# Kernel optimization log

Hardware: AMD Instinct MI355X
Metric: run time of the kernel (lower is better)

The kernel has to match this reference:

```python
import jax, jax.numpy as jnp
import numpy as np

B, L, D_MODEL = 2, 2048, 2048
D_INNER, D_STATE, D_CONV, DT_RANK = 4096, 16, 4, 128


def setup_inputs() -> dict:
    key = jax.random.key(0)
    ks = jax.random.split(key, 8)
    s = 0.02
    return {
        "hidden_states": jax.random.normal(ks[0], (B, L, D_MODEL), jnp.float32),
        "in_proj_weight": jax.random.normal(ks[1], (2 * D_INNER, D_MODEL), jnp.float32) * s,
        "conv1d_weight": jax.random.normal(ks[2], (D_INNER, 1, D_CONV), jnp.float32) * s,
        "conv1d_bias": jnp.zeros((D_INNER,), jnp.float32),
        "x_proj_weight": jax.random.normal(ks[3], (DT_RANK + 2 * D_STATE, D_INNER), jnp.float32) * s,
        "dt_proj_weight": jax.random.normal(ks[4], (D_INNER, DT_RANK), jnp.float32) * s,
        "dt_proj_bias": jax.random.uniform(ks[5], (D_INNER,), jnp.float32, -4.0, -2.0),
        "out_proj_weight": jax.random.normal(ks[6], (D_MODEL, D_INNER), jnp.float32) * s,
        # real Mamba init: A_log = log(1..d_state) broadcast over channels
        "A_log": jnp.log(jnp.broadcast_to(jnp.arange(1, D_STATE + 1, dtype=jnp.float32), (D_INNER, D_STATE))),
        "D": jnp.ones((D_INNER,), jnp.float32),
    }


def reference(hidden_states, in_proj_weight, conv1d_weight, conv1d_bias,
              x_proj_weight, dt_proj_weight, dt_proj_bias, out_proj_weight,
              A_log, D):
    negA = -jnp.exp(A_log)  # [d_inner, d_state]
    # in_proj (no bias) then transpose(1,2): [B, 2*d_inner, L]
    xz = jnp.einsum('bld,ed->bel', hidden_states, in_proj_weight)
    x, z = jnp.split(xz, 2, axis=1)  # each [B, d_inner, L]
    # causal depthwise conv1d + silu
    x = jax.lax.conv_general_dilated(
        x, conv1d_weight, window_strides=(1,), padding=[(D_CONV - 1, 0)],
        dimension_numbers=('NCH', 'OIH', 'NCH'), feature_group_count=D_INNER,
    ) + conv1d_bias[None, :, None]
    x = jax.nn.silu(x)
    xT = x.transpose(0, 2, 1)  # [B, L, d_inner]
    # x_proj -> (dt_rank, d_state, d_state)
    x_dbl = jnp.einsum('bld,ed->ble', xT, x_proj_weight)
    dt_lo = x_dbl[..., :DT_RANK]
    Bm = x_dbl[..., DT_RANK:DT_RANK + D_STATE]   # [B, L, n]
    Cm = x_dbl[..., DT_RANK + D_STATE:]          # [B, L, n]
    # dt_proj + delta_bias, softplus (delta_softplus=True)
    dt = jax.nn.softplus(jnp.einsum('blr,dr->bld', dt_lo, dt_proj_weight) + dt_proj_bias)

    # selective scan: h_t = exp(dt_t*A)*h_{t-1} + dt_t*x_t*B_t ; y_t = C_t . h_t
    def step(h, inp):
        dt_t, B_t, C_t, x_t = inp  # [B,d],[B,n],[B,n],[B,d]
        dA = jnp.exp(dt_t[..., None] * negA)           # [B, d, n]
        h = h * dA + (dt_t * x_t)[..., None] * B_t[:, None, :]
        y = jnp.einsum('bdn,bn->bd', h, C_t)
        return h, y

    h0 = jnp.zeros((B, D_INNER, D_STATE), dt.dtype)
    _, ys = jax.lax.scan(
        step, h0,
        (dt.transpose(1, 0, 2), Bm.transpose(1, 0, 2),
         Cm.transpose(1, 0, 2), xT.transpose(1, 0, 2)),
    )  # ys: [L, B, d_inner]
    y = ys.transpose(1, 0, 2) + xT * D          # skip connection D*x
    y = y * jax.nn.silu(z.transpose(0, 2, 1))   # gate
    # out_proj (no bias): [B, L, d_model]
    return jnp.einsum('bld,ed->ble', y, out_proj_weight)
```

## Files before the change

kernel.cpp:

```cpp
#include <hip/hip_runtime.h>
#include <math.h>

#define B_ 2
#define L_ 2048
#define DMODEL 2048
#define DINNER 4096
#define DSTATE 16
#define DCONV 4
#define DTRANK 128
#define NCHUNK 32
#define CLEN 64
#define MROWS 4096

typedef unsigned short ushort_t;
typedef unsigned int uint_t;
typedef __attribute__((ext_vector_type(8))) short bf16x8;
typedef __attribute__((ext_vector_type(4))) float floatx4;

__device__ __forceinline__ float sigmoidf_(float x){ return 1.f/(1.f+__expf(-x)); }
__device__ __forceinline__ ushort_t f2bf(float f){
    uint_t u = __builtin_bit_cast(uint_t, f);
    return (ushort_t)((u + 0x7FFFu + ((u >> 16) & 1u)) >> 16);
}
__device__ __forceinline__ float bf2f(ushort_t h){
    return __builtin_bit_cast(float, (uint_t)h << 16);
}
__device__ __forceinline__ float fast_exp2(float x){
#if __has_builtin(__builtin_amdgcn_exp2f)
    return __builtin_amdgcn_exp2f(x);
#else
    return exp2f(x);
#endif
}
#define LOG2E 1.44269504088896f

#define GLD_LDS16(g, l) __builtin_amdgcn_global_load_lds( \
    (const __attribute__((address_space(1))) void*)(g),   \
    (__attribute__((address_space(3))) void*)(l), 16, 0, 0)

template<int OUTBF, int EPI, int SPLIT, int KSPLIT>
__global__ __launch_bounds__(256)
void gemm_mfma(const ushort_t* __restrict__ Aptr, int lda,
               const ushort_t* __restrict__ W, int ldw,
               void* __restrict__ Cptr, void* __restrict__ C2,
               int ldc, int Klen,
               const float* __restrict__ bias)
{
    __shared__ ushort_t lsA[128*64];
    __shared__ ushort_t lsW[128*64];
    const int tid  = threadIdx.x;
    const int row0 = blockIdx.x * 128;
    const int col0 = blockIdx.y * 128;
    const int koff = KSPLIT ? blockIdx.z * Klen : 0;
    const int lane = tid & 63;
    const int wv   = tid >> 6;
    const int wm   = (wv >> 1) * 64;
    const int wn   = (wv & 1) * 64;
    const int lr   = lane & 15;
    const int lq   = lane >> 4;

    floatx4 acc[4][4];
    #pragma unroll
    for(int i=0;i<4;i++)
        #pragma unroll
        for(int j=0;j<4;j++)
            #pragma unroll
            for(int r=0;r<4;r++) acc[i][j][r] = 0.f;

    for(int k0 = koff; k0 < koff + Klen; k0 += 64){
        #pragma unroll
        for(int it=0; it<4; it++){
            const int slot = it*256 + tid;
            const int row  = slot >> 3;
            const int p    = slot & 7;
            const int s    = p ^ (row & 7);
            const ushort_t* gw = W    + (size_t)(col0 + row)*ldw + k0 + s*8;
            const ushort_t* ga = Aptr + (size_t)(row0 + row)*lda + k0 + s*8;
            GLD_LDS16(gw, &lsW[slot*8]);
            GLD_LDS16(ga, &lsA[slot*8]);
        }
        __syncthreads();

        #pragma unroll
        for(int kk=0; kk<2; kk++){
            bf16x8 af[4], bw[4];
            #pragma unroll
            for(int i=0;i<4;i++){
                const int ra = wm + i*16 + lr;
                const int rb = wn + i*16 + lr;
                af[i] = *(const bf16x8*)&lsA[ra*64 + (((kk*4+lq) ^ (ra&7))*8)];
                bw[i] = *(const bf16x8*)&lsW[rb*64 + (((kk*4+lq) ^ (rb&7))*8)];
            }
            #pragma unroll
            for(int i=0;i<4;i++)
                #pragma unroll
                for(int j=0;j<4;j++)
                    acc[i][j] = __builtin_amdgcn_mfma_f32_16x16x32_bf16(af[i], bw[j], acc[i][j], 0, 0, 0);
        }
        __syncthreads();
    }

    void* dst = Cptr;
    int cbase = col0;
    if (SPLIT && col0 >= ldc){ dst = C2; cbase = col0 - ldc; }
    const size_t zoff = KSPLIT ? (size_t)blockIdx.z * MROWS * ldc : 0;

    #pragma unroll
    for(int i=0;i<4;i++){
        #pragma unroll
        for(int r=0;r<4;r++){
            const int row = row0 + wm + i*16 + lq*4 + r;
            #pragma unroll
            for(int j=0;j<4;j++){
                const int col = cbase + wn + j*16 + lr;
                float v = acc[i][j][r];
                if (EPI){
                    v += bias[col];
                    v = (v > 20.f) ? v : log1pf(expf(v));
                }
                if (OUTBF) ((ushort_t*)dst)[(size_t)row*ldc + col] = f2bf(v);
                else       ((float*)  dst)[zoff + (size_t)row*ldc + col] = v;
            }
        }
    }
}

template<int OUTBF, int SPLIT, int KSPLIT>
__global__ __launch_bounds__(512, 2)
void gemm_256(const ushort_t* __restrict__ Aptr, int lda,
              const ushort_t* __restrict__ W, int ldw,
              void* __restrict__ Cptr, void* __restrict__ C2,
              int ldc, int Klen)
{
    __shared__ ushort_t lds[2][2][2][8192];
    const int tid  = threadIdx.x;
    const int row0 = blockIdx.x * 256;
    const int col0 = blockIdx.y * 256;
    const int koff = KSPLIT ? blockIdx.z * Klen : 0;
    const int NT   = Klen >> 6;
    const int lane = tid & 63;
    const int wv   = tid >> 6;
    const int wr   = wv >> 2;
    const int wc   = wv & 3;
    const int lr   = lane & 15;
    const int lq   = lane >> 4;

    int sdst0, sdst1;
    const ushort_t *aS0, *aS1, *wS0, *wS1;
    {
        const int g0 = tid,     dr0 = g0 >> 3, f0 = g0 & 7;
        const int g1 = 512+tid, dr1 = g1 >> 3, f1 = g1 & 7;
        const int u0 = f0 ^ (dr0 & 7), u1 = f1 ^ (dr1 & 7);
        const int r0s = dr0*2 + (u0 >> 2), c0s = (u0 & 3)*8;
        const int r1s = dr1*2 + (u1 >> 2), c1s = (u1 & 3)*8;
        sdst0 = g0*8; sdst1 = g1*8;
        aS0 = Aptr + (size_t)(row0 + r0s)*lda + c0s;
        aS1 = Aptr + (size_t)(row0 + r1s)*lda + c1s;
        wS0 = W    + (size_t)(col0 + r0s)*ldw + c0s;
        wS1 = W    + (size_t)(col0 + r1s)*ldw + c1s;
    }
    #define STG_A(kc, reg) { GLD_LDS16(aS0 + (kc), &(reg)[sdst0]); \
                             GLD_LDS16(aS1 + (kc), &(reg)[sdst1]); }
    #define STG_W(kc, reg) { GLD_LDS16(wS0 + (kc), &(reg)[sdst0]); \
                             GLD_LDS16(wS1 + (kc), &(reg)[sdst1]); }

    const int frd = ((lr & 1)*4 + lq) ^ (lr >> 1);
    const int aA  = (wr*64 + (lr >> 1))*64 + frd*8;
    const int aB  = (wc*32 + (lr >> 1))*64 + frd*8;

    floatx4 acc[8][4];
    #pragma unroll
    for(int i=0;i<8;i++)
        #pragma unroll
        for(int j=0;j<4;j++)
            #pragma unroll
            for(int r=0;r<4;r++) acc[i][j][r] = 0.f;

    STG_A(koff,    lds[0][0][0]);
    STG_W(koff,    lds[0][1][0]);
    STG_A(koff+32, lds[0][0][1]);
    STG_W(koff+32, lds[0][1][1]);
    STG_A(koff+64, lds[1][0][0]);
    STG_W(koff+64, lds[1][1][0]);
    asm volatile("s_waitcnt vmcnt(8)\ns_barrier" ::: "memory");

    for(int t=0; t<NT; ++t){
        const int c = t & 1;
        const ushort_t* cA0 = lds[c][0][0];
        const ushort_t* cB0 = lds[c][1][0];
        const ushort_t* cA1 = lds[c][0][1];
        const ushort_t* cB1 = lds[c][1][1];
        const int kt1 = koff + (t+1)*64;
        const int kt2 = koff + (t+2)*64;
        bf16x8 bw[4], af[8];

        #pragma unroll
        for(int j=0;j<4;j++) bw[j] = *(const bf16x8*)&cB0[aB + j*512];
        #pragma unroll
        for(int i=0;i<8;i++) af[i] = *(const bf16x8*)&cA0[aA + i*512];
        if (t+1 < NT){
            STG_A(kt1+32, lds[c^1][0][1]);
            STG_W(kt1+32, lds[c^1][1][1]);
        }
        __builtin_amdgcn_s_setprio(1);
        #pragma unroll
        for(int i=0;i<8;i++)
            #pragma unroll
            for(int j=0;j<4;j++)
                acc[i][j] = __builtin_amdgcn_mfma_f32_16x16x32_bf16(af[i], bw[j], acc[i][j],0,0,0);
        __builtin_amdgcn_s_setprio(0);
        if (t+1 < NT) asm volatile("s_waitcnt vmcnt(8)\ns_barrier" ::: "memory");
        else          asm volatile("s_waitcnt vmcnt(0)\ns_barrier" ::: "memory");

        #pragma unroll
        for(int j=0;j<4;j++) bw[j] = *(const bf16x8*)&cB1[aB + j*512];
        #pragma unroll
        for(int i=0;i<8;i++) af[i] = *(const bf16x8*)&cA1[aA + i*512];
        if (t+2 < NT){
            STG_A(kt2, lds[c][0][0]);
            STG_W(kt2, lds[c][1][0]);
        }
        __builtin_amdgcn_s_setprio(1);
        #pragma unroll
        for(int i=0;i<8;i++)
            #pragma unroll
            for(int j=0;j<4;j++)
                acc[i][j] = __builtin_amdgcn_mfma_f32_16x16x32_bf16(af[i], bw[j], acc[i][j],0,0,0);
        __builtin_amdgcn_s_setprio(0);
        if (t+2 < NT)      asm volatile("s_waitcnt vmcnt(8)\ns_barrier" ::: "memory");
        else if (t+1 < NT) asm volatile("s_waitcnt vmcnt(4)\ns_barrier" ::: "memory");
    }
    #undef STG_A
    #undef STG_W

    void* dst = Cptr;
    int cb = col0;
    if (SPLIT && col0 >= ldc){ dst = C2; cb = col0 - ldc; }
    const size_t zoff = KSPLIT ? (size_t)blockIdx.z * MROWS * ldc : 0;
    const int rbase = row0 + wr*128 + lq*4;
    const int cbase = cb + wc*64 + lr;
    #pragma unroll
    for(int i=0;i<8;i++){
        #pragma unroll
        for(int r=0;r<4;r++){
            const int row = rbase + i*16 + r;
            #pragma unroll
            for(int j=0;j<4;j++){
                const int col = cbase + j*16;
                const float v = acc[i][j][r];
                if (OUTBF) ((ushort_t*)dst)[(size_t)row*ldc + col] = f2bf(v);
                else       ((float*)dst)[zoff + (size_t)row*ldc + col] = v;
            }
        }
    }
}

__global__ __launch_bounds__(256)
void cvt_bf16(const float* __restrict__ in, ushort_t* __restrict__ out, int n4)
{
    const int i = blockIdx.x*256 + threadIdx.x;
    if (i < n4){
        float4 v = *(const float4*)(in + (size_t)i*4);
        union { ushort_t u[4]; uint2 q; } p;
        p.u[0]=f2bf(v.x); p.u[1]=f2bf(v.y); p.u[2]=f2bf(v.z); p.u[3]=f2bf(v.w);
        *(uint2*)(out + (size_t)i*4) = p.q;
    }
}

__global__ __launch_bounds__(256)
void cvt_pad256(const float* __restrict__ in, ushort_t* __restrict__ out)
{
    const int i = blockIdx.x*256 + threadIdx.x;
    const int row = i >> 10;
    const int c4  = i & 1023;
    union { ushort_t u[4]; uint2 q; } p;
    if (row < 160){
        float4 v = *(const float4*)(in + (size_t)row*4096 + c4*4);
        p.u[0]=f2bf(v.x); p.u[1]=f2bf(v.y); p.u[2]=f2bf(v.z); p.u[3]=f2bf(v.w);
    } else { p.u[0]=0; p.u[1]=0; p.u[2]=0; p.u[3]=0; }
    *(uint2*)(out + (size_t)i*4) = p.q;
}

__global__ __launch_bounds__(256)
void reduce_xproj(const float* __restrict__ P, float* __restrict__ xdbl,
                  ushort_t* __restrict__ dtlo)
{
    const int row = blockIdx.x;
    const int col = threadIdx.x;
    float s = 0.f;
    #pragma unroll
    for(int z=0; z<8; z++)
        s += P[(size_t)z*MROWS*256 + (size_t)row*256 + col];
    if (col < 160) xdbl[(size_t)row*160 + col] = s;
    if (col < DTRANK) dtlo[(size_t)row*DTRANK + col] = f2bf(s);
}

__global__ __launch_bounds__(256)
void conv_silu_bf(const ushort_t* __restrict__ xb, const float* __restrict__ w,
                  const float* __restrict__ bias, ushort_t* __restrict__ xc)
{
    const int gid = blockIdx.x*256 + threadIdx.x;
    const int d = gid & (DINNER-1);
    const int t = gid >> 12;
    const int l = t & (L_-1);
    float s = bias[d];
    #pragma unroll
    for(int j=0;j<DCONV;j++){
        const int ll = l - (DCONV-1) + j;
        if (ll >= 0)
            s = fmaf(bf2f(xb[(size_t)(t-(DCONV-1)+j)*DINNER + d]), w[d*DCONV+j], s);
    }
    xc[(size_t)t*DINNER + d] = f2bf(s * sigmoidf_(s));
}

__global__ __launch_bounds__(256)
void scan_phase1(const ushort_t* __restrict__ dt_bf,
                 const ushort_t* __restrict__ xconv,
                 const float* __restrict__ xdbl,
                 const float* __restrict__ A_log,
                 float* __restrict__ sc_h, float* __restrict__ sc_S)
{
    const int tid = threadIdx.x;
    const int d = blockIdx.x*256 + tid;
    const int chunk = blockIdx.y;
    const int b = blockIdx.z;
    const int l0 = chunk*CLEN;

    __shared__ float Bs[CLEN][DSTATE];
    for(int i=tid; i<CLEN*DSTATE; i+=256){
        const int row = i >> 4, n = i & 15;
        Bs[row][n] = xdbl[(size_t)(b*L_ + l0 + row)*160 + DTRANK + n];
    }
    float negA[DSTATE];
    #pragma unroll
    for(int n=0;n<DSTATE;n++) negA[n] = -expf(A_log[d*DSTATE + n]) * LOG2E;
    __syncthreads();

    float h[DSTATE], S[DSTATE];
    #pragma unroll
    for(int n=0;n<DSTATE;n++){ h[n]=0.f; S[n]=0.f; }

    size_t idx = (size_t)(b*L_ + l0)*DINNER + d;
    float dt_c = bf2f(dt_bf[idx]);
    float xv_c = bf2f(xconv[idx]);
    for(int l=0;l<CLEN;l++){
        float dt_n = 0.f, xv_n = 0.f;
        if (l+1 < CLEN){
            dt_n = bf2f(dt_bf[idx + DINNER]);
            xv_n = bf2f(xconv[idx + DINNER]);
        }
        const float dx = dt_c * xv_c;
        #pragma unroll
        for(int n=0;n<DSTATE;n++){
            const float t = dt_c * negA[n];
            S[n] += t;
            h[n] = fmaf(h[n], fast_exp2(t), dx*Bs[l][n]);
        }
        dt_c = dt_n; xv_c = xv_n;
        idx += DINNER;
    }
    const size_t o = (size_t)(b*NCHUNK + chunk)*DSTATE*DINNER + d;
    #pragma unroll
    for(int n=0;n<DSTATE;n++){
        sc_h[o + (size_t)n*DINNER] = h[n];
        sc_S[o + (size_t)n*DINNER] = S[n];
    }
}

__global__ __launch_bounds__(256)
void scan_phase2(float* __restrict__ sc_h, const float* __restrict__ sc_S)
{
    const int gid = blockIdx.x*256 + threadIdx.x;
    const int b = gid / (DSTATE*DINNER);
    const int rem = gid - b*DSTATE*DINNER;
    const size_t base = (size_t)b*NCHUNK*DSTATE*DINNER + rem;
    float H = 0.f;
    #pragma unroll
    for(int c=0;c<NCHUNK;c++){
        const size_t idx = base + (size_t)c*DSTATE*DINNER;
        const float he = sc_h[idx];
        const float S  = sc_S[idx];
        sc_h[idx] = H;
        H = fmaf(fast_exp2(S), H, he);
    }
}

__global__ __launch_bounds__(256)
void scan_phase3(const ushort_t* __restrict__ dt_bf,
                 const ushort_t* __restrict__ xconv,
                 const float* __restrict__ xdbl,
                 const ushort_t* __restrict__ z_bf,
                 const float* __restrict__ A_log,
                 const float* __restrict__ Dvec,
                 const float* __restrict__ sc_h,
                 ushort_t* __restrict__ y_bf)
{
    const int tid = threadIdx.x;
    const int d = blockIdx.x*256 + tid;
    const int chunk = blockIdx.y;
    const int b = blockIdx.z;
    const int l0 = chunk*CLEN;

    __shared__ float BCs[CLEN][2*DSTATE];
    for(int i=tid; i<CLEN*2*DSTATE; i+=256){
        const int row = i >> 5, c = i & 31;
        BCs[row][c] = xdbl[(size_t)(b*L_ + l0 + row)*160 + DTRANK + c];
    }
    float negA[DSTATE];
    #pragma unroll
    for(int n=0;n<DSTATE;n++) negA[n] = -expf(A_log[d*DSTATE + n]) * LOG2E;
    const float Dv = Dvec[d];
    float h[DSTATE];
    const size_t o = (size_t)(b*NCHUNK + chunk)*DSTATE*DINNER + d;
    #pragma unroll
    for(int n=0;n<DSTATE;n++) h[n] = sc_h[o + (size_t)n*DINNER];
    __syncthreads();

    size_t idx = (size_t)(b*L_ + l0)*DINNER + d;
    float dt_c = bf2f(dt_bf[idx]);
    float xv_c = bf2f(xconv[idx]);
    float zv_c = bf2f(z_bf[idx]);
    for(int l=0;l<CLEN;l++){
        float dt_n = 0.f, xv_n = 0.f, zv_n = 0.f;
        if (l+1 < CLEN){
            dt_n = bf2f(dt_bf[idx + DINNER]);
            xv_n = bf2f(xconv[idx + DINNER]);
            zv_n = bf2f(z_bf[idx + DINNER]);
        }
        const float dx = dt_c * xv_c;
        float y = 0.f;
        #pragma unroll
        for(int n=0;n<DSTATE;n++){
            const float t = dt_c * negA[n];
            h[n] = fmaf(h[n], fast_exp2(t), dx*BCs[l][n]);
            y = fmaf(h[n], BCs[l][DSTATE+n], y);
        }
        const float g = zv_c * sigmoidf_(zv_c);
        y_bf[idx] = f2bf(fmaf(xv_c, Dv, y) * g);
        dt_c = dt_n; xv_c = xv_n; zv_c = zv_n;
        idx += DINNER;
    }
}

extern "C" void kernel_launch(void* const* d_in, const int* in_sizes, int n_in,
                              void* d_out, int out_size, void* d_ws, size_t ws_size,
                              hipStream_t stream) {
    const float* hs      = (const float*)d_in[0];
    const float* w_in    = (const float*)d_in[1];
    const float* w_conv  = (const float*)d_in[2];
    const float* b_conv  = (const float*)d_in[3];
    const float* w_xproj = (const float*)d_in[4];
    const float* w_dt    = (const float*)d_in[5];
    const float* b_dt    = (const float*)d_in[6];
    const float* w_out   = (const float*)d_in[7];
    const float* A_log   = (const float*)d_in[8];
    const float* Dvec    = (const float*)d_in[9];
    float* out = (float*)d_out;

    char* base = (char*)d_ws;
    ushort_t* x_bf   = (ushort_t*)(base);
    float*    xdbl   = (float*)   (base);
    ushort_t* wx_bf  = (ushort_t*)(base + (4u<<20));
    ushort_t* dtlo_bf= (ushort_t*)(base + (6u<<20));
    ushort_t* wdt_bf = (ushort_t*)(base + (7u<<20));
    float*    sc_h   = (float*)   (base + (8u<<20));
    ushort_t* z_bf   = (ushort_t*)(base + (32u<<20));
    ushort_t* xconv  = (ushort_t*)(base + (64u<<20));
    ushort_t* wi_bf  = (ushort_t*)(base + (96u<<20));
    ushort_t* dt_bf  = (ushort_t*)(base + (96u<<20));
    ushort_t* hs_bf  = (ushort_t*)(base + (128u<<20));
    float*    sc_S   = (float*)   (base + (128u<<20));
    ushort_t* wo_bf  = (ushort_t*)(base + (128u<<20));
    float*    xp_par = (float*)   (base + (144u<<20));
    ushort_t* y_bf   = (ushort_t*)(base + (144u<<20));

    dim3 blk(256);
    dim3 blk5(512);

    cvt_bf16<<<dim3(MROWS*DMODEL/4/256), blk, 0, stream>>>(hs, hs_bf, MROWS*DMODEL/4);
    cvt_bf16<<<dim3(2*DINNER*DMODEL/4/256), blk, 0, stream>>>(w_in, wi_bf, 2*DINNER*DMODEL/4);

    gemm_256<1,1,0><<<dim3(MROWS/256, 2*DINNER/256), blk5, 0, stream>>>(
        hs_bf, DMODEL, wi_bf, DMODEL, x_bf, z_bf, DINNER, DMODEL);

    conv_silu_bf<<<dim3((size_t)MROWS*DINNER/256), blk, 0, stream>>>(x_bf, w_conv, b_conv, xconv);

    cvt_pad256<<<dim3(256*4096/4/256), blk, 0, stream>>>(w_xproj, wx_bf);
    gemm_mfma<0,0,0,1><<<dim3(MROWS/128, 2, 8), blk, 0, stream>>>(
        xconv, DINNER, wx_bf, DINNER, xp_par, nullptr, 256, DINNER/8, nullptr);
    reduce_xproj<<<dim3(MROWS), blk, 0, stream>>>(xp_par, xdbl, dtlo_bf);

    cvt_bf16<<<dim3(DINNER*DTRANK/4/256), blk, 0, stream>>>(w_dt, wdt_bf, DINNER*DTRANK/4);
    gemm_mfma<1,1,0,0><<<dim3(MROWS/128, DINNER/128), blk, 0, stream>>>(
        dtlo_bf, DTRANK, wdt_bf, DTRANK, dt_bf, nullptr, DINNER, DTRANK, b_dt);

    dim3 sgrid(DINNER/256, NCHUNK, B_);
    scan_phase1<<<sgrid, blk, 0, stream>>>(dt_bf, xconv, xdbl, A_log, sc_h, sc_S);
    scan_phase2<<<dim3(B_*DSTATE*DINNER/256), blk, 0, stream>>>(sc_h, sc_S);

    cvt_bf16<<<dim3(DMODEL*DINNER/4/256), blk, 0, stream>>>(w_out, wo_bf, DMODEL*DINNER/4);

    scan_phase3<<<sgrid, blk, 0, stream>>>(dt_bf, xconv, xdbl, z_bf, A_log, Dvec, sc_h, y_bf);

    gemm_mfma<0,0,0,0><<<dim3(MROWS/128, DMODEL/128), blk, 0, stream>>>(
        y_bf, DINNER, wo_bf, DINNER, out, nullptr, DMODEL, DINNER, nullptr);
}
```

Baseline: 669.8 us.

## Restructure GEMM main loop to full-tile double buffering with one barrier per iteration

Replaces the half-tile staggered prefetch, which had two barriers per K-step and fine-grained vmcnt waits, with a simpler scheme. Each iteration waits for all loads, issues the full next 64-wide K tile into the other buffer, and then computes both halves of the current buffer. Warp rows take the two halves in opposite order to spread LDS bank pressure. This halves barrier count but exposes more load latency, since each barrier waits with vmcnt(0) and prefetch distance is one full tile.

```diff
diff --git a/kernel.cpp b/kernel.cpp
--- a/kernel.cpp
+++ b/kernel.cpp
@@ -176,60 +176,47 @@
             #pragma unroll
             for(int r=0;r<4;r++) acc[i][j][r] = 0.f;
 
+    #define HALF_COMPUTE(cbuf, h) { \
+        const ushort_t* pA = lds[cbuf][0][h]; \
+        const ushort_t* pB = lds[cbuf][1][h]; \
+        bf16x8 af[8], bw[4]; \
+        _Pragma("unroll") \
+        for(int j=0;j<4;j++) bw[j] = *(const bf16x8*)&pB[aB + j*512]; \
+        _Pragma("unroll") \
+        for(int i=0;i<8;i++) af[i] = *(const bf16x8*)&pA[aA + i*512]; \
+        __builtin_amdgcn_s_setprio(1); \
+        _Pragma("unroll") \
+        for(int i=0;i<8;i++){ \
+            _Pragma("unroll") \
+            for(int j=0;j<4;j++) \
+                acc[i][j] = __builtin_amdgcn_mfma_f32_16x16x32_bf16(af[i], bw[j], acc[i][j],0,0,0); \
+        } \
+        __builtin_amdgcn_s_setprio(0); }
+
     STG_A(koff,    lds[0][0][0]);
+    STG_A(koff+32, lds[0][0][1]);
     STG_W(koff,    lds[0][1][0]);
-    STG_A(koff+32, lds[0][0][1]);
     STG_W(koff+32, lds[0][1][1]);
-    STG_A(koff+64, lds[1][0][0]);
-    STG_W(koff+64, lds[1][1][0]);
-    asm volatile("s_waitcnt vmcnt(8)\ns_barrier" ::: "memory");
 
     for(int t=0; t<NT; ++t){
         const int c = t & 1;
-        const ushort_t* cA0 = lds[c][0][0];
-        const ushort_t* cB0 = lds[c][1][0];
-        const ushort_t* cA1 = lds[c][0][1];
-        const ushort_t* cB1 = lds[c][1][1];
-        const int kt1 = koff + (t+1)*64;
-        const int kt2 = koff + (t+2)*64;
-        bf16x8 bw[4], af[8];
-
-        #pragma unroll
-        for(int j=0;j<4;j++) bw[j] = *(const bf16x8*)&cB0[aB + j*512];
-        #pragma unroll
-        for(int i=0;i<8;i++) af[i] = *(const bf16x8*)&cA0[aA + i*512];
+        asm volatile("s_waitcnt vmcnt(0)\ns_barrier" ::: "memory");
+        const int kn = koff + (t+1)*64;
         if (t+1 < NT){
-            STG_A(kt1+32, lds[c^1][0][1]);
-            STG_W(kt1+32, lds[c^1][1][1]);
-        }
-        __builtin_amdgcn_s_setprio(1);
-        #pragma unroll
-        for(int i=0;i<8;i++)
-            #pragma unroll
-            for(int j=0;j<4;j++)
-                acc[i][j] = __builtin_amdgcn_mfma_f32_16x16x32_bf16(af[i], bw[j], acc[i][j],0,0,0);
-        __builtin_amdgcn_s_setprio(0);
-        if (t+1 < NT) asm volatile("s_waitcnt vmcnt(8)\ns_barrier" ::: "memory");
-        else          asm volatile("s_waitcnt vmcnt(0)\ns_barrier" ::: "memory");
-
-        #pragma unroll
-        for(int j=0;j<4;j++) bw[j] = *(const bf16x8*)&cB1[aB + j*512];
-        #pragma unroll
-        for(int i=0;i<8;i++) af[i] = *(const bf16x8*)&cA1[aA + i*512];
-        if (t+2 < NT){
-            STG_A(kt2, lds[c][0][0]);
-            STG_W(kt2, lds[c][1][0]);
-        }
-        __builtin_amdgcn_s_setprio(1);
-        #pragma unroll
-        for(int i=0;i<8;i++)
-            #pragma unroll
-            for(int j=0;j<4;j++)
-                acc[i][j] = __builtin_amdgcn_mfma_f32_16x16x32_bf16(af[i], bw[j], acc[i][j],0,0,0);
-        __builtin_amdgcn_s_setprio(0);
-        if (t+2 < NT)      asm volatile("s_waitcnt vmcnt(8)\ns_barrier" ::: "memory");
-        else if (t+1 < NT) asm volatile("s_waitcnt vmcnt(4)\ns_barrier" ::: "memory");
-    }
+            STG_A(kn,    lds[c^1][0][0]);
+            STG_A(kn+32, lds[c^1][0][1]);
+            STG_W(kn,    lds[c^1][1][0]);
+            STG_W(kn+32, lds[c^1][1][1]);
+        }
+        if (wr == 0){
+            HALF_COMPUTE(c, 0);
+            HALF_COMPUTE(c, 1);
+        } else {
+            HALF_COMPUTE(c, 1);
+            HALF_COMPUTE(c, 0);
+        }
+    }
+    #undef HALF_COMPUTE
     #undef STG_A
     #undef STG_W
 
```

After: 658.9 us. Within noise of the previous version (-1.6%).

## Simplify GEMM LDS pipeline to whole-tile double buffering with one barrier

Applied to the files above, without the earlier changes.

Replaces the staggered half-tile prefetch schedule with plain double buffering. Each iteration waits for all loads, issues the next full K tile into the other buffer, reads both halves of the current tile from LDS, then runs all MFMAs. This drops to one barrier per iteration and gives the compiler one large MFMA block. The cost is a full vmcnt(0) wait before every iteration, so global-load latency is less hidden, and more registers are needed to hold both fragment sets at once.

```diff
diff --git a/kernel.cpp b/kernel.cpp
--- a/kernel.cpp
+++ b/kernel.cpp
@@ -177,58 +177,46 @@
             for(int r=0;r<4;r++) acc[i][j][r] = 0.f;
 
     STG_A(koff,    lds[0][0][0]);
+    STG_A(koff+32, lds[0][0][1]);
     STG_W(koff,    lds[0][1][0]);
-    STG_A(koff+32, lds[0][0][1]);
     STG_W(koff+32, lds[0][1][1]);
-    STG_A(koff+64, lds[1][0][0]);
-    STG_W(koff+64, lds[1][1][0]);
-    asm volatile("s_waitcnt vmcnt(8)\ns_barrier" ::: "memory");
 
     for(int t=0; t<NT; ++t){
         const int c = t & 1;
-        const ushort_t* cA0 = lds[c][0][0];
-        const ushort_t* cB0 = lds[c][1][0];
-        const ushort_t* cA1 = lds[c][0][1];
-        const ushort_t* cB1 = lds[c][1][1];
-        const int kt1 = koff + (t+1)*64;
-        const int kt2 = koff + (t+2)*64;
-        bf16x8 bw[4], af[8];
-
-        #pragma unroll
-        for(int j=0;j<4;j++) bw[j] = *(const bf16x8*)&cB0[aB + j*512];
-        #pragma unroll
-        for(int i=0;i<8;i++) af[i] = *(const bf16x8*)&cA0[aA + i*512];
+        asm volatile("s_waitcnt vmcnt(0)\ns_barrier" ::: "memory");
+        const int kn = koff + (t+1)*64;
         if (t+1 < NT){
-            STG_A(kt1+32, lds[c^1][0][1]);
-            STG_W(kt1+32, lds[c^1][1][1]);
-        }
+            STG_A(kn,    lds[c^1][0][0]);
+            STG_A(kn+32, lds[c^1][0][1]);
+            STG_W(kn,    lds[c^1][1][0]);
+            STG_W(kn+32, lds[c^1][1][1]);
+        }
+        const ushort_t* pA0 = lds[c][0][0];
+        const ushort_t* pB0 = lds[c][1][0];
+        const ushort_t* pA1 = lds[c][0][1];
+        const ushort_t* pB1 = lds[c][1][1];
+        bf16x8 a0[8], b0v[4], a1[8], b1v[4];
+        #pragma unroll
+        for(int j=0;j<4;j++) b0v[j] = *(const bf16x8*)&pB0[aB + j*512];
+        #pragma unroll
+        for(int i=0;i<8;i++) a0[i]  = *(const bf16x8*)&pA0[aA + i*512];
+        #pragma unroll
+        for(int j=0;j<4;j++) b1v[j] = *(const bf16x8*)&pB1[aB + j*512];
+        #pragma unroll
+        for(int i=0;i<8;i++) a1[i]  = *(const bf16x8*)&pA1[aA + i*512];
+        __builtin_amdgcn_sched_barrier(0);
         __builtin_amdgcn_s_setprio(1);
         #pragma unroll
         for(int i=0;i<8;i++)
             #pragma unroll
             for(int j=0;j<4;j++)
-                acc[i][j] = __builtin_amdgcn_mfma_f32_16x16x32_bf16(af[i], bw[j], acc[i][j],0,0,0);
+                acc[i][j] = __builtin_amdgcn_mfma_f32_16x16x32_bf16(a0[i], b0v[j], acc[i][j],0,0,0);
+        #pragma unroll
+        for(int i=0;i<8;i++)
+            #pragma unroll
+            for(int j=0;j<4;j++)
+                acc[i][j] = __builtin_amdgcn_mfma_f32_16x16x32_bf16(a1[i], b1v[j], acc[i][j],0,0,0);
         __builtin_amdgcn_s_setprio(0);
-        if (t+1 < NT) asm volatile("s_waitcnt vmcnt(8)\ns_barrier" ::: "memory");
-        else          asm volatile("s_waitcnt vmcnt(0)\ns_barrier" ::: "memory");
-
-        #pragma unroll
-        for(int j=0;j<4;j++) bw[j] = *(const bf16x8*)&cB1[aB + j*512];
-        #pragma unroll
-        for(int i=0;i<8;i++) af[i] = *(const bf16x8*)&cA1[aA + i*512];
-        if (t+2 < NT){
-            STG_A(kt2, lds[c][0][0]);
-            STG_W(kt2, lds[c][1][0]);
-        }
-        __builtin_amdgcn_s_setprio(1);
-        #pragma unroll
-        for(int i=0;i<8;i++)
-            #pragma unroll
-            for(int j=0;j<4;j++)
-                acc[i][j] = __builtin_amdgcn_mfma_f32_16x16x32_bf16(af[i], bw[j], acc[i][j],0,0,0);
-        __builtin_amdgcn_s_setprio(0);
-        if (t+2 < NT)      asm volatile("s_waitcnt vmcnt(8)\ns_barrier" ::: "memory");
-        else if (t+1 < NT) asm volatile("s_waitcnt vmcnt(4)\ns_barrier" ::: "memory");
     }
     #undef STG_A
     #undef STG_W
```

After: 670.5 us. No clear change (+0.1%).
